# Kernel tuning notes

Hardware: AMD Instinct MI355X
Metric: run time of the kernel (lower is better)

## Reference

```python
import jax, jax.numpy as jnp
import numpy as np

# (pt, eta, phi) feature indices per particle for each block (eta=None for MET)
A_PT, A_ETA, A_PHI = [5, 4, 35, 34], [9, 8, 45, 44], [13, 12, 55, 54]            # e3,e2,j9,j8
B_PT, B_ETA, B_PHI = [3, 33, 31, 2], [7, 43, 41, 6], [11, 53, 51, 10]            # e1,j7,j5,e0
C_PT, C_ETA, C_PHI = [28, 32, 15, 16], [38, 42, 19, 20], [48, 52, 23, 24]        # j2,j6,mu1,mu2
D_PT, D_ETA, D_PHI = [0, 14, 30, 26, 29, 27, 17], [None, 18, 40, 36, 39, 37, 21], [1, 22, 50, 46, 49, 47, 25]  # MET,mu0,j4,j0,j3,j1,mu3


def _bc(a, nd):
    # broadcast a (B,) or () angle factor over nd trailing qubit axes
    return a.reshape(a.shape + (1,) * nd)


def _rx(state, theta, w):
    nd = state.ndim - 2
    c = _bc(jnp.cos(theta * 0.5), nd)
    s = _bc(jnp.sin(theta * 0.5), nd)
    s0 = jnp.take(state, 0, axis=w + 1)
    s1 = jnp.take(state, 1, axis=w + 1)
    return jnp.stack([c * s0 - 1j * s * s1, -1j * s * s0 + c * s1], axis=w + 1)


def _ry(state, theta, w):
    nd = state.ndim - 2
    c = _bc(jnp.cos(theta * 0.5), nd)
    s = _bc(jnp.sin(theta * 0.5), nd)
    s0 = jnp.take(state, 0, axis=w + 1)
    s1 = jnp.take(state, 1, axis=w + 1)
    return jnp.stack([c * s0 - s * s1, s * s0 + c * s1], axis=w + 1)


def _rz(state, theta, w):
    nd = state.ndim - 2
    ph = _bc(jnp.exp(-0.5j * theta.astype(state.dtype)), nd)
    s0 = jnp.take(state, 0, axis=w + 1)
    s1 = jnp.take(state, 1, axis=w + 1)
    return jnp.stack([ph * s0, jnp.conj(ph) * s1], axis=w + 1)


def _cnot(state, ctrl, tgt):
    c0 = jnp.take(state, 0, axis=ctrl + 1)
    c1 = jnp.take(state, 1, axis=ctrl + 1)
    t_ax = tgt + 1 if tgt < ctrl else tgt  # ctrl axis removed shifts higher wires down
    c1 = jnp.flip(c1, axis=t_ax)
    return jnp.stack([c0, c1], axis=ctrl + 1)


def _extract(x, pt_idx, eta_idx, phi_idx):
    pt = x[:, np.array(pt_idx)]
    eta = jnp.stack([x[:, i] if i is not None else jnp.zeros(x.shape[0], x.dtype) for i in eta_idx], axis=1)
    phi = x[:, np.array(phi_idx)]
    return pt, eta, phi


def _run_block(pt, eta, phi, weights, n, latent, trash, depth):
    B = pt.shape[0]
    state = jnp.zeros((B,) + (2,) * n, dtype=jnp.complex64)
    state = state.at[(slice(None),) + (0,) * n].set(1.0)
    for k in range(n):
        state = _rx(state, eta[:, k], k)
        state = _ry(state, pt[:, k], k)
        state = _rz(state, phi[:, k], k)
    for k in range(n - 1):
        state = _cnot(state, k, k + 1)
    for k in range(n):
        state = _rz(state, eta[:, k], k)
        state = _ry(state, pt[:, k], k)
        state = _rx(state, phi[:, k], k)
    for d in range(depth):
        for t in trash:
            for l in latent:
                state = _cnot(state, t, l)
        for k in range(n):
            state = _ry(state, weights[d * n + k], k)
        for l in latent:
            for t in trash:
                state = _cnot(state, l, t)
    p = jnp.abs(state) ** 2  # (B, 2,...,2) real probabilities
    red = tuple(range(1, n))
    zs = [jnp.sum(jnp.take(p, 0, axis=w + 1), axis=red) - jnp.sum(jnp.take(p, 1, axis=w + 1), axis=red) for w in trash]
    return jnp.stack(zs, axis=1)


def setup_inputs() -> dict:
    key = jax.random.key(0)
    k0, k1, k2, k3, k4 = jax.random.split(key, 5)
    B = 131072
    x = jax.random.normal(k0, (B, 56), dtype=jnp.float32)
    wA = 0.01 * jax.random.normal(k1, (4,), dtype=jnp.float32)
    wB = 0.01 * jax.random.normal(k2, (4,), dtype=jnp.float32)
    wC = 0.01 * jax.random.normal(k3, (4,), dtype=jnp.float32)
    wD = 0.01 * jax.random.normal(k4, (28,), dtype=jnp.float32)
    return {"x": x, "wA": wA, "wB": wB, "wC": wC, "wD": wD}


def reference(x, wA, wB, wC, wD):
    zA = _run_block(*_extract(x, A_PT, A_ETA, A_PHI), wA, 4, (0, 1), (2, 3), 1)  # (B,2)
    zB = _run_block(*_extract(x, B_PT, B_ETA, B_PHI), wB, 4, (0, 1), (2, 3), 1)  # (B,2)
    zC = _run_block(*_extract(x, C_PT, C_ETA, C_PHI), wC, 4, (0, 1), (2, 3), 1)  # (B,2)
    zD = _run_block(*_extract(x, D_PT, D_ETA, D_PHI), wD, 7, (0, 1, 2, 3), (4, 5, 6), 4)  # (B,3)
    return jnp.concatenate([zA, zB, zC, zD], axis=1)  # (B,9) ~ dict values concatenated
```

## Files before the change

kernel.cpp:

```cpp
#include <hip/hip_runtime.h>
#include <hip/hip_fp16.h>


#define DEVINL __device__ __forceinline__

typedef _Float16 hv2 __attribute__((ext_vector_type(2)));

struct C2 { __half2 rr, mp; };

DEVINL C2 mkc(float re, float im) {
  C2 c; c.rr = __floats2half2_rn(re, re); c.mp = __floats2half2_rn(-im, im); return c;
}
DEVINL __half2 mkamp(float re, float im) { return __floats2half2_rn(re, im); }
DEVINL __half2 swap2(__half2 v) { return __lowhigh2highlow(v); }
DEVINL __half2 cmulc(C2 u, __half2 v) { return __hfma2(u.rr, v, __hmul2(u.mp, swap2(v))); }

DEVINL float ampsq(__half2 v, float acc) {
#if __has_builtin(__builtin_amdgcn_fdot2)
  return __builtin_amdgcn_fdot2(__builtin_bit_cast(hv2, v), __builtin_bit_cast(hv2, v), acc, false);
#else
  float2 f = __half22float2(v);
  return fmaf(f.x, f.x, fmaf(f.y, f.y, acc));
#endif
}

constexpr int parc(int x) { x ^= x >> 4; x ^= x >> 2; x ^= x >> 1; return x & 1; }

struct c32 { float x, y; };
DEVINL c32 cmulf(c32 a, c32 b) { return { a.x*b.x - a.y*b.y, a.x*b.y + a.y*b.x }; }

DEVINL __half2 lx1(__half2 v) {
  int q = __shfl_xor(__builtin_bit_cast(int, v), 1, 64);
  return __builtin_bit_cast(__half2, q);
}
DEVINL float lx1f(float v) { return __shfl_xor(v, 1, 64); }


template<int N, int W>
DEVINL void g_ry(__half2* a, __half2 c2, __half2 s2, __half2 ns2) {
  constexpr int M = 1 << (N - 1 - W);
#pragma unroll
  for (int i = 0; i < (1 << N); ++i) if (!(i & M)) {
    const int j = i | M;
    __half2 v0 = a[i], v1 = a[j];
    a[i] = __hfma2(c2, v0, __hmul2(ns2, v1));
    a[j] = __hfma2(c2, v1, __hmul2(s2, v0));
  }
}

template<int N, int W>
DEVINL void g_u2(__half2* a, C2 u00, C2 u01, C2 u10, C2 u11) {
  constexpr int M = 1 << (N - 1 - W);
#pragma unroll
  for (int i = 0; i < (1 << N); ++i) if (!(i & M)) {
    const int j = i | M;
    __half2 v0 = a[i], v1 = a[j], v0s = swap2(v0), v1s = swap2(v1);
    a[i] = __hfma2(u00.rr, v0, __hfma2(u00.mp, v0s, __hfma2(u01.rr, v1, __hmul2(u01.mp, v1s))));
    a[j] = __hfma2(u10.rr, v0, __hfma2(u10.mp, v0s, __hfma2(u11.rr, v1, __hmul2(u11.mp, v1s))));
  }
}

template<int N, int C, int T>
DEVINL void g_cnot(__half2* a) {
  constexpr int CM = 1 << (N - 1 - C), TM = 1 << (N - 1 - T);
#pragma unroll
  for (int i = 0; i < (1 << N); ++i) if ((i & CM) && !(i & TM)) {
    const int j = i | TM;
    __half2 t = a[i]; a[i] = a[j]; a[j] = t;
  }
}

template<int N, int K>
DEVINL void chain_cnot(__half2* a) {
  if constexpr (K < N - 1) { g_cnot<N, K, K + 1>(a); chain_cnot<N, K + 1>(a); }
}


DEVINL void mk_u01(float ce, float se, float cp, float sp, float cf, float sf,
                   c32& u0, c32& u1) {
  u0 = cmulf({cf, -sf}, {cp * ce, sp * se});
  u1 = cmulf({cf,  sf}, {sp * ce, -cp * se});
}

DEVINL void mk_U(float ce, float se, float cp, float sp, float cf, float sf,
                 C2& U00, C2& U01, C2& U10, C2& U11) {
  c32 z = {ce, -se}, zb = {ce, se};
  c32 A = cmulf({cf * cp, -sf * sp}, z);
  c32 T = cmulf({cf * sp,  sf * cp}, zb);
  c32 Cc = cmulf({cf * sp, -sf * cp}, z);
  c32 D = cmulf({cf * cp,  sf * sp}, zb);
  U00 = mkc(A.x, A.y); U01 = mkc(-T.x, -T.y); U10 = mkc(Cc.x, Cc.y); U11 = mkc(D.x, D.y);
}

DEVINL void load_sc(const float* __restrict__ xr, int eta_i, int pt_i, int phi_i,
                    float& ce, float& se, float& cp, float& sp, float& cf, float& sf) {
  float e = (eta_i < 0) ? 0.f : xr[eta_i];
  __sincosf(0.5f * e, &se, &ce);
  __sincosf(0.5f * xr[pt_i], &sp, &cp);
  __sincosf(0.5f * xr[phi_i], &sf, &cf);
}

template<int N, int M, class CF>
DEVINL void build_rec(__half2* a, CF cf) {
  if constexpr (M < N) {
    c32 u0, u1; cf(M, u0, u1);
    C2 c0 = mkc(u0.x, u0.y), c1 = mkc(u1.x, u1.y);
#pragma unroll
    for (int j = (1 << M) - 1; j >= 0; --j) {
      __half2 s = a[j];
      a[2 * j]     = cmulc(c0, s);
      a[2 * j + 1] = cmulc(c1, s);
    }
    build_rec<N, M + 1>(a, cf);
  }
}

template<int N, int K, class CF>
DEVINL void usweep_rec(__half2* a, CF cf) {
  if constexpr (K < N) {
    C2 U00, U01, U10, U11;
    cf(K, U00, U01, U10, U11);
    g_u2<N, K>(a, U00, U01, U10, U11);
    usweep_rec<N, K + 1>(a, cf);
  }
}

template<int N, int K, class CF>
DEVINL void ry_rec(__half2* a, CF cf) {
  if constexpr (K < N) {
    __half2 c2, s2, ns2;
    cf(K, c2, s2, ns2);
    g_ry<N, K>(a, c2, s2, ns2);
    ry_rec<N, K + 1>(a, cf);
  }
}


template<int I>
DEVINL void sim4h(const float* __restrict__ xr, const float* __restrict__ w, float* z) {
  constexpr int PT[3][4]  = {{5, 4, 35, 34}, {3, 33, 31, 2}, {28, 32, 15, 16}};
  constexpr int ETA[3][4] = {{9, 8, 45, 44}, {7, 43, 41, 6}, {38, 42, 19, 20}};
  constexpr int PHI[3][4] = {{13, 12, 55, 54}, {11, 53, 51, 10}, {48, 52, 23, 24}};
  __half2 a[16];
  a[0] = mkamp(1.f, 0.f);
  build_rec<4, 0>(a, [&](int M, c32& u0, c32& u1) {
    float ce, se, cp, sp, cf, sf;
    load_sc(xr, ETA[I][M], PT[I][M], PHI[I][M], ce, se, cp, sp, cf, sf);
    mk_u01(ce, se, cp, sp, cf, sf, u0, u1);
  });
  chain_cnot<4, 0>(a);
  usweep_rec<4, 0>(a, [&](int K, C2& U00, C2& U01, C2& U10, C2& U11) {
    float ce, se, cp, sp, cf, sf;
    load_sc(xr, ETA[I][K], PT[I][K], PHI[I][K], ce, se, cp, sp, cf, sf);
    mk_U(ce, se, cp, sp, cf, sf, U00, U01, U10, U11);
  });

#pragma unroll
  for (int i = 0; i < 16; ++i)
    if (parc(i & 3) && !(i & 8)) { __half2 t = a[i]; a[i] = a[i ^ 12]; a[i ^ 12] = t; }

  ry_rec<4, 0>(a, [&](int K, __half2& c2, __half2& s2, __half2& ns2) {
    float sv, cv; __sincosf(0.5f * w[K], &sv, &cv);
    c2 = __floats2half2_rn(cv, cv);
    s2 = __floats2half2_rn(sv, sv);
    ns2 = __floats2half2_rn(-sv, -sv);
  });

#pragma unroll
  for (int i = 0; i < 16; ++i)
    if (parc(i & 12) && !(i & 2)) { __half2 t = a[i]; a[i] = a[i ^ 3]; a[i ^ 3] = t; }

  float cls[4];
#pragma unroll
  for (int c = 0; c < 4; ++c) cls[c] = 0.f;
#pragma unroll
  for (int i = 0; i < 16; ++i) cls[i & 3] = ampsq(a[i], cls[i & 3]);
  float z0 = 0.f, z1 = 0.f;
#pragma unroll
  for (int c = 0; c < 4; ++c) {
    z0 += (c & 2) ? -cls[c] : cls[c];
    z1 += (c & 1) ? -cls[c] : cls[c];
  }
  z[0] = z0; z[1] = z1;
}


DEVINL void role4(const float* __restrict__ x,
                  const float* __restrict__ wA, const float* __restrict__ wB,
                  const float* __restrict__ wC,
                  float* __restrict__ out, int B, int s, int rb) {
  const int b = rb * 256 + threadIdx.x;
  if (b >= B) return;
  const float* xr = x + (size_t)b * 56;

  float o[2];
  if (s == 0)      sim4h<0>(xr, wA, o);
  else if (s == 1) sim4h<1>(xr, wB, o);
  else             sim4h<2>(xr, wC, o);

  float* op = out + (size_t)b * 9 + 2 * s;
  op[0] = o[0]; op[1] = o[1];
}

DEVINL void role7(const float* __restrict__ x, const float* __restrict__ wD,
                  float* __restrict__ out, int B, int rb) {
  const int t = rb * 256 + threadIdx.x;
  const int b = t >> 1;
  if (b >= B) return;
  const bool po = (t & 1) != 0;

  constexpr int PT[7]  = {0, 14, 30, 26, 29, 27, 17};
  constexpr int ETA[7] = {-1, 18, 40, 36, 39, 37, 21};
  constexpr int PHI[7] = {1, 22, 50, 46, 49, 47, 25};

  const float* xr = x + (size_t)b * 56;

  __half2 a[64];
  a[0] = mkamp(1.f, 0.f);
  build_rec<6, 0>(a, [&](int M, c32& u0, c32& u1) {
    const int k = M + 1;
    float ce, se, cp, sp, cf, sf;
    load_sc(xr, ETA[k], PT[k], PHI[k], ce, se, cp, sp, cf, sf);
    mk_u01(ce, se, cp, sp, cf, sf, u0, u1);
  });
  {
    float ce, se, cp, sp, cf, sf;
    load_sc(xr, ETA[0], PT[0], PHI[0], ce, se, cp, sp, cf, sf);
    c32 u0, u1; mk_u01(ce, se, cp, sp, cf, sf, u0, u1);
    C2 c0 = mkc(po ? u1.x : u0.x, po ? u1.y : u0.y);
#pragma unroll
    for (int i = 0; i < 64; ++i) a[i] = cmulc(c0, a[i]);
  }

#pragma unroll
  for (int i = 0; i < 32; ++i) {
    const int j = i | 32;
    __half2 t0 = po ? a[j] : a[i];
    __half2 t1 = po ? a[i] : a[j];
    a[i] = t0; a[j] = t1;
  }
  chain_cnot<6, 0>(a);

  {
    float ce, se, cp, sp, cf, sf;
    load_sc(xr, ETA[0], PT[0], PHI[0], ce, se, cp, sp, cf, sf);
    C2 U00, U01, U10, U11;
    mk_U(ce, se, cp, sp, cf, sf, U00, U01, U10, U11);
    C2 UA, UB;
    UA.rr = po ? U11.rr : U00.rr; UA.mp = po ? U11.mp : U00.mp;
    UB.rr = po ? U10.rr : U01.rr; UB.mp = po ? U10.mp : U01.mp;
#pragma unroll
    for (int i = 0; i < 64; ++i) {
      __half2 m = a[i], q = lx1(m);
      a[i] = __hfma2(UA.rr, m, __hfma2(UA.mp, swap2(m),
             __hfma2(UB.rr, q, __hmul2(UB.mp, swap2(q)))));
    }
  }
  usweep_rec<6, 0>(a, [&](int W, C2& U00, C2& U01, C2& U10, C2& U11) {
    const int k = W + 1;
    float ce, se, cp, sp, cf, sf;
    load_sc(xr, ETA[k], PT[k], PHI[k], ce, se, cp, sp, cf, sf);
    mk_U(ce, se, cp, sp, cf, sf, U00, U01, U10, U11);
  });

#pragma unroll 1
  for (int d = 0; d < 4; ++d) {
#pragma unroll
    for (int i = 0; i < 64; ++i)
      if (parc(i & 7) && !(i & 0x20)) {
        const int j = i ^ 0x38;
        __half2 t0 = lx1(a[j]);
        __half2 t1 = lx1(a[i]);
        a[i] = t0; a[j] = t1;
      }

    {
      float sv, cv; __sincosf(0.5f * wD[7 * d], &sv, &cv);
      __half2 c2v = __floats2half2_rn(cv, cv);
      __half2 sp2 = __floats2half2_rn(po ? sv : -sv, po ? sv : -sv);
#pragma unroll
      for (int i = 0; i < 64; ++i) {
        __half2 q = lx1(a[i]);
        a[i] = __hfma2(c2v, a[i], __hmul2(sp2, q));
      }
    }
    ry_rec<6, 0>(a, [&](int W, __half2& c2, __half2& s2, __half2& ns2) {
      float sv, cv; __sincosf(0.5f * wD[7 * d + W + 1], &sv, &cv);
      c2 = __floats2half2_rn(cv, cv);
      s2 = __floats2half2_rn(sv, sv);
      ns2 = __floats2half2_rn(-sv, -sv);
    });

#pragma unroll
    for (int i = 0; i < 64; ++i)
      if (!(i & 4)) {
        const int j = i ^ 7;
        __half2 t0, t1;
        if (parc(i & 0x38)) { t0 = po ? a[i] : a[j]; t1 = po ? a[j] : a[i]; }
        else                { t0 = po ? a[j] : a[i]; t1 = po ? a[i] : a[j]; }
        a[i] = t0; a[j] = t1;
      }
  }

  float cls[8];
#pragma unroll
  for (int c = 0; c < 8; ++c) cls[c] = 0.f;
#pragma unroll
  for (int i = 0; i < 64; ++i) cls[i & 7] = ampsq(a[i], cls[i & 7]);
  float z4 = 0.f, z5 = 0.f, z6 = 0.f;
#pragma unroll
  for (int c = 0; c < 8; ++c) {
    z4 += (c & 4) ? -cls[c] : cls[c];
    z5 += (c & 2) ? -cls[c] : cls[c];
    z6 += (c & 1) ? -cls[c] : cls[c];
  }
  z4 += lx1f(z4); z5 += lx1f(z5); z6 += lx1f(z6);
  if (!po) {
    float* op = out + (size_t)b * 9 + 6;
    op[0] = z4; op[1] = z5; op[2] = z6;
  }
}


__global__ void
__attribute__((amdgpu_flat_work_group_size(256, 256), amdgpu_waves_per_eu(4, 4)))
k_all(const float* __restrict__ x,
      const float* __restrict__ wA, const float* __restrict__ wB,
      const float* __restrict__ wC, const float* __restrict__ wD,
      float* __restrict__ out, int B, int gx) {
  const int bx = blockIdx.x;
  if (bx < 3 * gx) {
    const int s = (bx >= 2 * gx) ? 2 : (int)(bx >= gx);
    role4(x, wA, wB, wC, out, B, s, bx - s * gx);
  } else {
    role7(x, wD, out, B, bx - 3 * gx);
  }
}


extern "C" void kernel_launch(void* const* d_in, const int* in_sizes, int n_in,
                              void* d_out, int out_size, void* d_ws, size_t ws_size,
                              hipStream_t stream) {
  const float* x  = (const float*)d_in[0];
  const float* wA = (const float*)d_in[1];
  const float* wB = (const float*)d_in[2];
  const float* wC = (const float*)d_in[3];
  const float* wD = (const float*)d_in[4];
  float* out = (float*)d_out;
  const int B = in_sizes[0] / 56;
  const int threads = 256;

  const int gx = (B + threads - 1) / threads;
  const int gy = (2 * B + threads - 1) / threads;
  k_all<<<3 * gx + gy, threads, 0, stream>>>(x, wA, wB, wC, wD, out, B, gx);
}
```

Measured before the change: 149.0 us.

## Split 7-qubit state across four lanes instead of two

The 7-qubit block now spreads each sample's 128-amplitude state over four lanes, with two qubits mapped to lane bits, so each thread holds 32 amplitudes instead of 64. Gates on the two lane qubits become cross-lane shuffles or selects, and the final reduction takes two shuffle steps. This lowers per-thread register pressure and raises thread-level parallelism, at the cost of twice as many threads for this role and extra shuffles. The launch attributes are also changed from explicit AMDGPU flat-work-group and waves-per-EU bounds to __launch_bounds__(256, 4).

Result: faster. 143.1 us (-4.0%).

```diff
diff --git a/kernel.cpp b/kernel.cpp
--- a/kernel.cpp
+++ b/kernel.cpp
@@ -29,11 +29,13 @@
 struct c32 { float x, y; };
 DEVINL c32 cmulf(c32 a, c32 b) { return { a.x*b.x - a.y*b.y, a.x*b.y + a.y*b.x }; }
 
-DEVINL __half2 lx1(__half2 v) {
-  int q = __shfl_xor(__builtin_bit_cast(int, v), 1, 64);
+template<int K>
+DEVINL __half2 lxk(__half2 v) {
+  int q = __shfl_xor(__builtin_bit_cast(int, v), K, 64);
   return __builtin_bit_cast(__half2, q);
 }
-DEVINL float lx1f(float v) { return __shfl_xor(v, 1, 64); }
+template<int K>
+DEVINL float lxkf(float v) { return __shfl_xor(v, K, 64); }
 
 
 template<int N, int W>
@@ -205,9 +207,11 @@
 DEVINL void role7(const float* __restrict__ x, const float* __restrict__ wD,
                   float* __restrict__ out, int B, int rb) {
   const int t = rb * 256 + threadIdx.x;
-  const int b = t >> 1;
+  const int b = t >> 2;
   if (b >= B) return;
-  const bool po = (t & 1) != 0;
+  const int sub = t & 3;
+  const bool b0 = (sub & 2) != 0;
+  const bool b1 = (sub & 1) != 0;
 
   constexpr int PT[7]  = {0, 14, 30, 26, 29, 27, 17};
   constexpr int ETA[7] = {-1, 18, 40, 36, 39, 37, 21};
@@ -215,10 +219,10 @@
 
   const float* xr = x + (size_t)b * 56;
 
-  __half2 a[64];
+  __half2 a[32];
   a[0] = mkamp(1.f, 0.f);
-  build_rec<6, 0>(a, [&](int M, c32& u0, c32& u1) {
-    const int k = M + 1;
+  build_rec<5, 0>(a, [&](int M, c32& u0, c32& u1) {
+    const int k = M + 2;
     float ce, se, cp, sp, cf, sf;
     load_sc(xr, ETA[k], PT[k], PHI[k], ce, se, cp, sp, cf, sf);
     mk_u01(ce, se, cp, sp, cf, sf, u0, u1);
@@ -226,20 +230,30 @@
   {
     float ce, se, cp, sp, cf, sf;
     load_sc(xr, ETA[0], PT[0], PHI[0], ce, se, cp, sp, cf, sf);
-    c32 u0, u1; mk_u01(ce, se, cp, sp, cf, sf, u0, u1);
-    C2 c0 = mkc(po ? u1.x : u0.x, po ? u1.y : u0.y);
-#pragma unroll
-    for (int i = 0; i < 64; ++i) a[i] = cmulc(c0, a[i]);
+    c32 q0u0, q0u1; mk_u01(ce, se, cp, sp, cf, sf, q0u0, q0u1);
+    load_sc(xr, ETA[1], PT[1], PHI[1], ce, se, cp, sp, cf, sf);
+    c32 q1u0, q1u1; mk_u01(ce, se, cp, sp, cf, sf, q1u0, q1u1);
+    c32 f0 = b0 ? q0u1 : q0u0;
+    c32 f1 = b1 ? q1u1 : q1u0;
+    c32 f = cmulf(f0, f1);
+    C2 cf2 = mkc(f.x, f.y);
+#pragma unroll
+    for (int i = 0; i < 32; ++i) a[i] = cmulc(cf2, a[i]);
   }
 
 #pragma unroll
   for (int i = 0; i < 32; ++i) {
-    const int j = i | 32;
-    __half2 t0 = po ? a[j] : a[i];
-    __half2 t1 = po ? a[i] : a[j];
-    a[i] = t0; a[j] = t1;
-  }
-  chain_cnot<6, 0>(a);
+    __half2 q = lxk<1>(a[i]);
+    a[i] = b0 ? q : a[i];
+  }
+#pragma unroll
+  for (int i = 0; i < 16; ++i) {
+    const int j = i | 16;
+    __half2 lo = a[i], hi = a[j];
+    a[i] = b1 ? hi : lo;
+    a[j] = b1 ? lo : hi;
+  }
+  chain_cnot<5, 0>(a);
 
   {
     float ce, se, cp, sp, cf, sf;
@@ -247,17 +261,32 @@
     C2 U00, U01, U10, U11;
     mk_U(ce, se, cp, sp, cf, sf, U00, U01, U10, U11);
     C2 UA, UB;
-    UA.rr = po ? U11.rr : U00.rr; UA.mp = po ? U11.mp : U00.mp;
-    UB.rr = po ? U10.rr : U01.rr; UB.mp = po ? U10.mp : U01.mp;
-#pragma unroll
-    for (int i = 0; i < 64; ++i) {
-      __half2 m = a[i], q = lx1(m);
+    UA.rr = b0 ? U11.rr : U00.rr; UA.mp = b0 ? U11.mp : U00.mp;
+    UB.rr = b0 ? U10.rr : U01.rr; UB.mp = b0 ? U10.mp : U01.mp;
+#pragma unroll
+    for (int i = 0; i < 32; ++i) {
+      __half2 m = a[i], q = lxk<2>(m);
       a[i] = __hfma2(UA.rr, m, __hfma2(UA.mp, swap2(m),
              __hfma2(UB.rr, q, __hmul2(UB.mp, swap2(q)))));
     }
   }
-  usweep_rec<6, 0>(a, [&](int W, C2& U00, C2& U01, C2& U10, C2& U11) {
-    const int k = W + 1;
+  {
+    float ce, se, cp, sp, cf, sf;
+    load_sc(xr, ETA[1], PT[1], PHI[1], ce, se, cp, sp, cf, sf);
+    C2 U00, U01, U10, U11;
+    mk_U(ce, se, cp, sp, cf, sf, U00, U01, U10, U11);
+    C2 UA, UB;
+    UA.rr = b1 ? U11.rr : U00.rr; UA.mp = b1 ? U11.mp : U00.mp;
+    UB.rr = b1 ? U10.rr : U01.rr; UB.mp = b1 ? U10.mp : U01.mp;
+#pragma unroll
+    for (int i = 0; i < 32; ++i) {
+      __half2 m = a[i], q = lxk<1>(m);
+      a[i] = __hfma2(UA.rr, m, __hfma2(UA.mp, swap2(m),
+             __hfma2(UB.rr, q, __hmul2(UB.mp, swap2(q)))));
+    }
+  }
+  usweep_rec<5, 0>(a, [&](int W, C2& U00, C2& U01, C2& U10, C2& U11) {
+    const int k = W + 2;
     float ce, se, cp, sp, cf, sf;
     load_sc(xr, ETA[k], PT[k], PHI[k], ce, se, cp, sp, cf, sf);
     mk_U(ce, se, cp, sp, cf, sf, U00, U01, U10, U11);
@@ -266,47 +295,60 @@
 #pragma unroll 1
   for (int d = 0; d < 4; ++d) {
 #pragma unroll
-    for (int i = 0; i < 64; ++i)
-      if (parc(i & 7) && !(i & 0x20)) {
-        const int j = i ^ 0x38;
-        __half2 t0 = lx1(a[j]);
-        __half2 t1 = lx1(a[i]);
+    for (int i = 0; i < 32; ++i)
+      if (parc(i & 7) && !(i & 0x10)) {
+        const int j = i ^ 0x18;
+        __half2 t0 = lxk<3>(a[j]);
+        __half2 t1 = lxk<3>(a[i]);
         a[i] = t0; a[j] = t1;
       }
 
     {
       float sv, cv; __sincosf(0.5f * wD[7 * d], &sv, &cv);
       __half2 c2v = __floats2half2_rn(cv, cv);
-      __half2 sp2 = __floats2half2_rn(po ? sv : -sv, po ? sv : -sv);
-#pragma unroll
-      for (int i = 0; i < 64; ++i) {
-        __half2 q = lx1(a[i]);
-        a[i] = __hfma2(c2v, a[i], __hmul2(sp2, q));
+      __half2 se2 = __floats2half2_rn(b0 ? sv : -sv, b0 ? sv : -sv);
+#pragma unroll
+      for (int i = 0; i < 32; ++i) {
+        __half2 q = lxk<2>(a[i]);
+        a[i] = __hfma2(c2v, a[i], __hmul2(se2, q));
       }
     }
-    ry_rec<6, 0>(a, [&](int W, __half2& c2, __half2& s2, __half2& ns2) {
-      float sv, cv; __sincosf(0.5f * wD[7 * d + W + 1], &sv, &cv);
+    {
+      float sv, cv; __sincosf(0.5f * wD[7 * d + 1], &sv, &cv);
+      __half2 c2v = __floats2half2_rn(cv, cv);
+      __half2 se2 = __floats2half2_rn(b1 ? sv : -sv, b1 ? sv : -sv);
+#pragma unroll
+      for (int i = 0; i < 32; ++i) {
+        __half2 q = lxk<1>(a[i]);
+        a[i] = __hfma2(c2v, a[i], __hmul2(se2, q));
+      }
+    }
+    ry_rec<5, 0>(a, [&](int W, __half2& c2, __half2& s2, __half2& ns2) {
+      float sv, cv; __sincosf(0.5f * wD[7 * d + W + 2], &sv, &cv);
       c2 = __floats2half2_rn(cv, cv);
       s2 = __floats2half2_rn(sv, sv);
       ns2 = __floats2half2_rn(-sv, -sv);
     });
 
-#pragma unroll
-    for (int i = 0; i < 64; ++i)
-      if (!(i & 4)) {
-        const int j = i ^ 7;
-        __half2 t0, t1;
-        if (parc(i & 0x38)) { t0 = po ? a[i] : a[j]; t1 = po ? a[j] : a[i]; }
-        else                { t0 = po ? a[j] : a[i]; t1 = po ? a[i] : a[j]; }
-        a[i] = t0; a[j] = t1;
-      }
+    {
+      const bool ps = b0 ^ b1;
+#pragma unroll
+      for (int i = 0; i < 32; ++i)
+        if (!(i & 4)) {
+          const int j = i ^ 7;
+          const bool cond = parc(i & 0x18) ? !ps : ps;
+          __half2 lo = a[i], hi = a[j];
+          a[i] = cond ? hi : lo;
+          a[j] = cond ? lo : hi;
+        }
+    }
   }
 
   float cls[8];
 #pragma unroll
   for (int c = 0; c < 8; ++c) cls[c] = 0.f;
 #pragma unroll
-  for (int i = 0; i < 64; ++i) cls[i & 7] = ampsq(a[i], cls[i & 7]);
+  for (int i = 0; i < 32; ++i) cls[i & 7] = ampsq(a[i], cls[i & 7]);
   float z4 = 0.f, z5 = 0.f, z6 = 0.f;
 #pragma unroll
   for (int c = 0; c < 8; ++c) {
@@ -314,16 +356,16 @@
     z5 += (c & 2) ? -cls[c] : cls[c];
     z6 += (c & 1) ? -cls[c] : cls[c];
   }
-  z4 += lx1f(z4); z5 += lx1f(z5); z6 += lx1f(z6);
-  if (!po) {
+  z4 += lxkf<1>(z4); z5 += lxkf<1>(z5); z6 += lxkf<1>(z6);
+  z4 += lxkf<2>(z4); z5 += lxkf<2>(z5); z6 += lxkf<2>(z6);
+  if (sub == 0) {
     float* op = out + (size_t)b * 9 + 6;
     op[0] = z4; op[1] = z5; op[2] = z6;
   }
 }
 
 
-__global__ void
-__attribute__((amdgpu_flat_work_group_size(256, 256), amdgpu_waves_per_eu(4, 4)))
+__global__ void __launch_bounds__(256, 4)
 k_all(const float* __restrict__ x,
       const float* __restrict__ wA, const float* __restrict__ wB,
       const float* __restrict__ wC, const float* __restrict__ wD,
@@ -351,6 +393,6 @@
   const int threads = 256;
 
   const int gx = (B + threads - 1) / threads;
-  const int gy = (2 * B + threads - 1) / threads;
+  const int gy = (4 * B + threads - 1) / threads;
   k_all<<<3 * gx + gy, threads, 0, stream>>>(x, wA, wB, wC, wD, out, B, gx);
 }
```
